# Kernel tuning notes

Hardware: AMD Instinct MI355X
Metric: run time of the kernel (lower is better)

Reference implementation:

```python
import jax, jax.numpy as jnp
import numpy as np

N = 50000      # nodes
C = 64         # in_channels
O = 64         # out_channels (== in_channels, required by zeros_like in original)
S = 8          # size: number of weight matrices
E = 1700000    # edges (neighbor pairs incl. self-loops), avg degree ~34


def setup_inputs() -> dict:
    key = jax.random.key(0)
    ks = jax.random.split(key, 9)
    node_tensor = jax.random.normal(ks[0], (N, C), dtype=jnp.float32)
    src = jax.random.randint(ks[1], (E,), 0, N)                 # neighbor node j
    dst = jnp.sort(jax.random.randint(ks[2], (E,), 0, N))       # center node i
    sc = 1.0 / np.sqrt(C)
    W = jax.random.normal(ks[3], (S, C, O), dtype=jnp.float32) * sc   # linears weights
    b = jax.random.normal(ks[4], (S, O), dtype=jnp.float32) * sc      # linears biases
    Ws = jax.random.normal(ks[5], (C, S), dtype=jnp.float32) * sc     # source proj
    bs = jax.random.normal(ks[6], (S,), dtype=jnp.float32) * sc
    Wt = jax.random.normal(ks[7], (C, S), dtype=jnp.float32) * sc     # target proj
    bt = jax.random.normal(ks[8], (S,), dtype=jnp.float32) * sc
    return dict(node_tensor=node_tensor, src=src, dst=dst,
                W=W, b=b, Ws=Ws, bs=bs, Wt=Wt, bt=bt)


def reference(node_tensor, src, dst, W, b, Ws, bs, Wt, bt):
    # Per-node soft-assignment logits (FeaStNet)
    s = node_tensor @ Ws + bs          # [N, S] : source_tensor
    t = node_tensor @ Wt + bt          # [N, S] : target_tensor
    # Per-edge assignment: softmax over the `size` dim of source[center] + target[neighbor]
    q = jax.nn.softmax(s[dst] + t[src], axis=-1)      # [E, S]
    # Per-matrix projected node features: weighted[m] = x @ W_m + b_m
    Wx = jnp.einsum('nc,sco->sno', node_tensor, W) + b[:, None, :]   # [S, N, O]
    # msg[e] = sum_m q[e,m] * Wx[m, src[e]]; loop over small fixed S to avoid [S,E,O] blowup
    msg = q[:, 0:1] * Wx[0][src]                      # [E, O]
    for m in range(1, S):
        msg = msg + q[:, m:m + 1] * Wx[m][src]
    # Scatter-sum over each center's neighborhood, mean over the S weight matrices
    out = jax.ops.segment_sum(msg, dst, num_segments=N) / S          # [N, O]
    return out
```

## Files before the change

### kernel.cpp

```cpp
#include <hip/hip_runtime.h>
#include <hip/hip_bf16.h>


#define CDIM 64
#define SDIM 8

typedef __bf16 bf16x8 __attribute__((ext_vector_type(8)));
typedef float f32x4 __attribute__((ext_vector_type(4)));

__global__ __launch_bounds__(256) void k1_pre(
    const float* __restrict__ x, const float* __restrict__ Ws,
    const float* __restrict__ bs, const float* __restrict__ Wt,
    const float* __restrict__ bt, const float* __restrict__ W,
    const int* __restrict__ dst, float* __restrict__ ST,
    __hip_bfloat16* __restrict__ xbf, __hip_bfloat16* __restrict__ WtB,
    int* __restrict__ rowptr, int N, int E, int nbN) {
  int bid = blockIdx.x;
  if (bid >= nbN + 128) {
    int e = (bid - nbN - 128) * 256 + threadIdx.x;
    if (e >= E) return;
    int a = dst[e];
    int bnd = (e + 1 < E) ? dst[e + 1] : N;
    if (e == 0) {
      for (int d = 0; d <= a; ++d) rowptr[d] = 0;
    }
    for (int d = a + 1; d <= bnd; ++d) rowptr[d] = e + 1;
    return;
  }
  if (bid >= nbN) {
    int t = (bid - nbN) * 256 + threadIdx.x;
    int o = t >> 9, k = t & 511;
    WtB[t] = __float2bfloat16(W[(size_t)k * 64 + o]);
    return;
  }

  __shared__ __hip_bfloat16 wst[16 * 72];
  __shared__ float bst[16];
  int t = threadIdx.x;
#pragma unroll
  for (int j = 0; j < 4; ++j) {
    int idx = t * 4 + j;
    int n = idx >> 6, k = idx & 63;
    float v = (n < 8) ? Ws[k * 8 + n] : Wt[k * 8 + (n - 8)];
    wst[n * 72 + k] = __float2bfloat16(v);
  }
  if (t < 16) bst[t] = (t < 8) ? bs[t] : bt[t - 8];
  __syncthreads();

  int wave = t >> 6, lane = t & 63;
  int r = lane & 15, q = lane >> 4;
  int node = bid * 64 + wave * 16 + r;
  int nodec = node < N ? node : N - 1;
  const float* xr = x + (size_t)nodec * CDIM;

  bf16x8 afrag[2];
#pragma unroll
  for (int kt = 0; kt < 2; ++kt) {
    float4 u0 = *(const float4*)(xr + kt * 32 + q * 8);
    float4 u1 = *(const float4*)(xr + kt * 32 + q * 8 + 4);
    union { bf16x8 v; __hip_bfloat16 h[8]; } a;
    a.h[0] = __float2bfloat16(u0.x); a.h[1] = __float2bfloat16(u0.y);
    a.h[2] = __float2bfloat16(u0.z); a.h[3] = __float2bfloat16(u0.w);
    a.h[4] = __float2bfloat16(u1.x); a.h[5] = __float2bfloat16(u1.y);
    a.h[6] = __float2bfloat16(u1.z); a.h[7] = __float2bfloat16(u1.w);
    afrag[kt] = a.v;
    if (node < N)
      *(bf16x8*)(xbf + (size_t)node * CDIM + kt * 32 + q * 8) = a.v;
  }

  bf16x8 bf0 = *(const bf16x8*)(wst + r * 72 + q * 8);
  bf16x8 bf1 = *(const bf16x8*)(wst + r * 72 + 32 + q * 8);

  f32x4 acc = {0, 0, 0, 0};
  acc = __builtin_amdgcn_mfma_f32_16x16x32_bf16(afrag[0], bf0, acc, 0, 0, 0);
  acc = __builtin_amdgcn_mfma_f32_16x16x32_bf16(afrag[1], bf1, acc, 0, 0, 0);

  int m = lane & 15;
#pragma unroll
  for (int v = 0; v < 4; ++v) {
    int nd = bid * 64 + wave * 16 + q * 4 + v;
    if (nd >= N) continue;
    float val = acc[v] + bst[m];
    if (m >= 8) val = __expf(val);
    ST[nd * 16 + m] = val;
  }
}

__global__ __launch_bounds__(256) void k3_fused(
    const __hip_bfloat16* __restrict__ xbf, const int* __restrict__ src,
    const int* __restrict__ rowptr, const float* __restrict__ ST,
    __hip_bfloat16* __restrict__ Gbf, float* __restrict__ R, int N) {
  __shared__ float qlds[4][64];
  int wave = __builtin_amdgcn_readfirstlane(threadIdx.x >> 6);
  int lane = threadIdx.x & 63;
  int i = blockIdx.x * 4 + wave;
  if (i >= N) return;

  int lo = rowptr[i];
  int hi = rowptr[i + 1];
  int mm = lane & 7;
  int kk = lane >> 3;

  float uv = __expf(ST[i * 16 + mm]);

  float g[8] = {0, 0, 0, 0, 0, 0, 0, 0};
  float racc = 0.f;
  float* qw = &qlds[wave][0];

  if (lo < hi) {
    int ecl = hi - 1;
    int ek = lo + kk;
    int iv = src[ek < ecl ? ek : ecl];

    for (int e0 = lo; e0 < hi; e0 += 8) {
      int e0n = e0 + 8;
      int ekn = e0n + kk;
      int ivn = (e0n < hi) ? src[ekn < ecl ? ekn : ecl] : iv;

      int j0 = __builtin_amdgcn_readlane(iv, 0);
      int j1 = __builtin_amdgcn_readlane(iv, 8);
      int j2 = __builtin_amdgcn_readlane(iv, 16);
      int j3 = __builtin_amdgcn_readlane(iv, 24);
      int j4 = __builtin_amdgcn_readlane(iv, 32);
      int j5 = __builtin_amdgcn_readlane(iv, 40);
      int j6 = __builtin_amdgcn_readlane(iv, 48);
      int j7 = __builtin_amdgcn_readlane(iv, 56);

      float tv = ST[iv * 16 + 8 + mm];

      float xv[8];
      xv[0] = __bfloat162float(xbf[(size_t)j0 * CDIM + lane]);
      xv[1] = __bfloat162float(xbf[(size_t)j1 * CDIM + lane]);
      xv[2] = __bfloat162float(xbf[(size_t)j2 * CDIM + lane]);
      xv[3] = __bfloat162float(xbf[(size_t)j3 * CDIM + lane]);
      xv[4] = __bfloat162float(xbf[(size_t)j4 * CDIM + lane]);
      xv[5] = __bfloat162float(xbf[(size_t)j5 * CDIM + lane]);
      xv[6] = __bfloat162float(xbf[(size_t)j6 * CDIM + lane]);
      xv[7] = __bfloat162float(xbf[(size_t)j7 * CDIM + lane]);

      float w = uv * tv;
      float ssum = w + __shfl_xor(w, 1);
      ssum += __shfl_xor(ssum, 2);
      ssum += __shfl_xor(ssum, 4);
      float qv = w * __frcp_rn(ssum);
      if (e0 + kk >= hi) qv = 0.f;
      racc += qv;
      qw[lane] = qv;

#pragma unroll
      for (int k = 0; k < 8; ++k) {
        float4 qa = *(const float4*)(qw + k * 8);
        float4 qb = *(const float4*)(qw + k * 8 + 4);
        float xk = xv[k];
        g[0] = fmaf(qa.x, xk, g[0]);
        g[1] = fmaf(qa.y, xk, g[1]);
        g[2] = fmaf(qa.z, xk, g[2]);
        g[3] = fmaf(qa.w, xk, g[3]);
        g[4] = fmaf(qb.x, xk, g[4]);
        g[5] = fmaf(qb.y, xk, g[5]);
        g[6] = fmaf(qb.z, xk, g[6]);
        g[7] = fmaf(qb.w, xk, g[7]);
      }
      iv = ivn;
    }
  }

  __hip_bfloat16* Gi = Gbf + (size_t)i * 512;
#pragma unroll
  for (int m = 0; m < 8; ++m) Gi[m * 64 + lane] = __float2bfloat16(g[m]);

  racc += __shfl_xor(racc, 8);
  racc += __shfl_xor(racc, 16);
  racc += __shfl_xor(racc, 32);
  if (lane < 8) R[(size_t)i * 8 + lane] = racc;
}

__global__ __launch_bounds__(256) void k4_mfma(
    const __hip_bfloat16* __restrict__ Gbf, const float* __restrict__ R,
    const __hip_bfloat16* __restrict__ WtB, const float* __restrict__ bias,
    float* __restrict__ out, int N) {
  __shared__ float4 btile[64 * 65];
  {
    const float4* srcp = (const float4*)WtB;
    int t = threadIdx.x;
#pragma unroll
    for (int j = 0; j < 16; ++j) {
      int ci = t + j * 256;
      btile[(ci >> 6) * 65 + (ci & 63)] = srcp[ci];
    }
  }
  __syncthreads();

  int wave = threadIdx.x >> 6;
  int lane = threadIdx.x & 63;
  int r0 = (blockIdx.x * 4 + wave) * 16;
  if (r0 >= N) return;

  int m = lane & 15;
  int q = lane >> 4;
  const __bf16* abase = (const __bf16*)(Gbf + (size_t)(r0 + m) * 512) + q * 8;
  const __bf16* lbase = (const __bf16*)btile + (size_t)m * 520 + q * 8;

  f32x4 acc0 = {0, 0, 0, 0}, acc1 = {0, 0, 0, 0};
  f32x4 acc2 = {0, 0, 0, 0}, acc3 = {0, 0, 0, 0};
#pragma unroll
  for (int kt = 0; kt < 16; ++kt) {
    bf16x8 a = *(const bf16x8*)(abase + kt * 32);
    bf16x8 b0 = *(const bf16x8*)(lbase + 0 * 520 + kt * 32);
    bf16x8 b1 = *(const bf16x8*)(lbase + 16 * 520 + kt * 32);
    bf16x8 b2 = *(const bf16x8*)(lbase + 32 * 520 + kt * 32);
    bf16x8 b3 = *(const bf16x8*)(lbase + 48 * 520 + kt * 32);
    acc0 = __builtin_amdgcn_mfma_f32_16x16x32_bf16(a, b0, acc0, 0, 0, 0);
    acc1 = __builtin_amdgcn_mfma_f32_16x16x32_bf16(a, b1, acc1, 0, 0, 0);
    acc2 = __builtin_amdgcn_mfma_f32_16x16x32_bf16(a, b2, acc2, 0, 0, 0);
    acc3 = __builtin_amdgcn_mfma_f32_16x16x32_bf16(a, b3, acc3, 0, 0, 0);
  }

#pragma unroll
  for (int v = 0; v < 4; ++v) {
    int ri = r0 + q * 4 + v;
    if (ri >= N) continue;
    const float* Ri = R + (size_t)ri * 8;
    float b0s = 0, b1s = 0, b2s = 0, b3s = 0;
#pragma unroll
    for (int mm = 0; mm < 8; ++mm) {
      float rv = Ri[mm];
      b0s = fmaf(rv, bias[mm * 64 + 0 + m], b0s);
      b1s = fmaf(rv, bias[mm * 64 + 16 + m], b1s);
      b2s = fmaf(rv, bias[mm * 64 + 32 + m], b2s);
      b3s = fmaf(rv, bias[mm * 64 + 48 + m], b3s);
    }
    float* orow = out + (size_t)ri * 64;
    orow[0 + m]  = (acc0[v] + b0s) * 0.125f;
    orow[16 + m] = (acc1[v] + b1s) * 0.125f;
    orow[32 + m] = (acc2[v] + b2s) * 0.125f;
    orow[48 + m] = (acc3[v] + b3s) * 0.125f;
  }
}

extern "C" void kernel_launch(void* const* d_in, const int* in_sizes, int n_in,
                              void* d_out, int out_size, void* d_ws, size_t ws_size,
                              hipStream_t stream) {
  const float* x  = (const float*)d_in[0];
  const int* src  = (const int*)d_in[1];
  const int* dst  = (const int*)d_in[2];
  const float* W  = (const float*)d_in[3];
  const float* b  = (const float*)d_in[4];
  const float* Ws = (const float*)d_in[5];
  const float* bs = (const float*)d_in[6];
  const float* Wt = (const float*)d_in[7];
  const float* bt = (const float*)d_in[8];
  int N = in_sizes[0] / CDIM;
  int E = in_sizes[1];
  float* out = (float*)d_out;

  float* ST = (float*)d_ws;
  __hip_bfloat16* Gbf = (__hip_bfloat16*)(ST + (size_t)N * 16);
  float* R  = (float*)(Gbf + (size_t)N * 512);
  __hip_bfloat16* WtB = (__hip_bfloat16*)(R + (size_t)N * 8);
  __hip_bfloat16* xbf = WtB + 64 * 512;
  int* rowptr = (int*)(xbf + (size_t)N * CDIM);

  int nbN = (N + 63) / 64;
  int nbE = (E + 255) / 256;
  k1_pre<<<nbN + 128 + nbE, 256, 0, stream>>>(x, Ws, bs, Wt, bt, W, dst, ST,
                                              xbf, WtB, rowptr, N, E, nbN);
  k3_fused<<<(N + 3) / 4, 256, 0, stream>>>(xbf, src, rowptr, ST, Gbf, R, N);
  int mtiles = (N + 15) / 16;
  k4_mfma<<<(mtiles + 3) / 4, 256, 0, stream>>>(Gbf, R, WtB, b, out, N);
}
```

Measured before the change: 160.1 us.

## Compute per-node q^T·X aggregation with MFMA over 32-edge chunks

The gather-aggregation kernel now processes 32 edges per iteration. Each lane loads 8 contiguous bf16 channels per neighbor as a vector instead of scalar loads. The q weights and gathered x rows are staged in LDS as bf16 tiles, and the 8x64 per-node product is computed with 16x16x32 bf16 MFMA instead of scalar FMAs. This cuts ALU work and load instruction count, but adds LDS staging, a transposing scalar LDS read, and padding waste for low-degree nodes, with q rounded to bf16.

```diff
diff --git a/kernel.cpp b/kernel.cpp
--- a/kernel.cpp
+++ b/kernel.cpp
@@ -86,88 +86,115 @@
   }
 }
 
-__global__ __launch_bounds__(256) void k3_fused(
+__global__ __launch_bounds__(256) void k3_mfma(
     const __hip_bfloat16* __restrict__ xbf, const int* __restrict__ src,
     const int* __restrict__ rowptr, const float* __restrict__ ST,
     __hip_bfloat16* __restrict__ Gbf, float* __restrict__ R, int N) {
-  __shared__ float qlds[4][64];
-  int wave = __builtin_amdgcn_readfirstlane(threadIdx.x >> 6);
+  __shared__ __hip_bfloat16 qt_s[4][16 * 40];
+  __shared__ __hip_bfloat16 xt_s[4][32 * 72];
+
+  int wave = threadIdx.x >> 6;
   int lane = threadIdx.x & 63;
   int i = blockIdx.x * 4 + wave;
   if (i >= N) return;
 
+  int mm = lane & 7;
+  int kk = lane >> 3;
+  int mp = lane & 15;
+  int q3 = lane >> 4;
+
+  __hip_bfloat16* qt = &qt_s[wave][0];
+  __hip_bfloat16* xt = &xt_s[wave][0];
+
+  __hip_bfloat16 z0 = __float2bfloat16(0.0f);
+#pragma unroll
+  for (int z = 0; z < 5; ++z) qt[320 + z * 64 + lane] = z0;
+
   int lo = rowptr[i];
   int hi = rowptr[i + 1];
-  int mm = lane & 7;
-  int kk = lane >> 3;
-
   float uv = __expf(ST[i * 16 + mm]);
 
-  float g[8] = {0, 0, 0, 0, 0, 0, 0, 0};
+  f32x4 acc0 = {0, 0, 0, 0}, acc1 = {0, 0, 0, 0};
+  f32x4 acc2 = {0, 0, 0, 0}, acc3 = {0, 0, 0, 0};
   float racc = 0.f;
-  float* qw = &qlds[wave][0];
 
   if (lo < hi) {
     int ecl = hi - 1;
-    int ek = lo + kk;
-    int iv = src[ek < ecl ? ek : ecl];
-
-    for (int e0 = lo; e0 < hi; e0 += 8) {
-      int e0n = e0 + 8;
-      int ekn = e0n + kk;
-      int ivn = (e0n < hi) ? src[ekn < ecl ? ekn : ecl] : iv;
-
-      int j0 = __builtin_amdgcn_readlane(iv, 0);
-      int j1 = __builtin_amdgcn_readlane(iv, 8);
-      int j2 = __builtin_amdgcn_readlane(iv, 16);
-      int j3 = __builtin_amdgcn_readlane(iv, 24);
-      int j4 = __builtin_amdgcn_readlane(iv, 32);
-      int j5 = __builtin_amdgcn_readlane(iv, 40);
-      int j6 = __builtin_amdgcn_readlane(iv, 48);
-      int j7 = __builtin_amdgcn_readlane(iv, 56);
-
-      float tv = ST[iv * 16 + 8 + mm];
-
-      float xv[8];
-      xv[0] = __bfloat162float(xbf[(size_t)j0 * CDIM + lane]);
-      xv[1] = __bfloat162float(xbf[(size_t)j1 * CDIM + lane]);
-      xv[2] = __bfloat162float(xbf[(size_t)j2 * CDIM + lane]);
-      xv[3] = __bfloat162float(xbf[(size_t)j3 * CDIM + lane]);
-      xv[4] = __bfloat162float(xbf[(size_t)j4 * CDIM + lane]);
-      xv[5] = __bfloat162float(xbf[(size_t)j5 * CDIM + lane]);
-      xv[6] = __bfloat162float(xbf[(size_t)j6 * CDIM + lane]);
-      xv[7] = __bfloat162float(xbf[(size_t)j7 * CDIM + lane]);
-
-      float w = uv * tv;
-      float ssum = w + __shfl_xor(w, 1);
-      ssum += __shfl_xor(ssum, 2);
-      ssum += __shfl_xor(ssum, 4);
-      float qv = w * __frcp_rn(ssum);
-      if (e0 + kk >= hi) qv = 0.f;
-      racc += qv;
-      qw[lane] = qv;
-
-#pragma unroll
-      for (int k = 0; k < 8; ++k) {
-        float4 qa = *(const float4*)(qw + k * 8);
-        float4 qb = *(const float4*)(qw + k * 8 + 4);
-        float xk = xv[k];
-        g[0] = fmaf(qa.x, xk, g[0]);
-        g[1] = fmaf(qa.y, xk, g[1]);
-        g[2] = fmaf(qa.z, xk, g[2]);
-        g[3] = fmaf(qa.w, xk, g[3]);
-        g[4] = fmaf(qb.x, xk, g[4]);
-        g[5] = fmaf(qb.y, xk, g[5]);
-        g[6] = fmaf(qb.z, xk, g[6]);
-        g[7] = fmaf(qb.w, xk, g[7]);
+    int iv[4];
+#pragma unroll
+    for (int g = 0; g < 4; ++g) {
+      int ek = lo + g * 8 + kk;
+      iv[g] = src[ek < ecl ? ek : ecl];
+    }
+
+    for (int c0 = lo; c0 < hi; c0 += 32) {
+      bf16x8 xv[4];
+#pragma unroll
+      for (int g = 0; g < 4; ++g)
+        xv[g] = *(const bf16x8*)(xbf + (size_t)iv[g] * CDIM + mm * 8);
+
+      float tv[4];
+#pragma unroll
+      for (int g = 0; g < 4; ++g) tv[g] = ST[iv[g] * 16 + 8 + mm];
+
+      int nc0 = c0 + 32;
+      int niv[4];
+#pragma unroll
+      for (int g = 0; g < 4; ++g) {
+        int ek = nc0 + g * 8 + kk;
+        ek = ek < ecl ? ek : ecl;
+        niv[g] = (nc0 < hi) ? src[ek] : iv[g];
       }
-      iv = ivn;
-    }
-  }
-
-  __hip_bfloat16* Gi = Gbf + (size_t)i * 512;
-#pragma unroll
-  for (int m = 0; m < 8; ++m) Gi[m * 64 + lane] = __float2bfloat16(g[m]);
+
+#pragma unroll
+      for (int g = 0; g < 4; ++g) {
+        float w = uv * tv[g];
+        float ssum = w + __shfl_xor(w, 1);
+        ssum += __shfl_xor(ssum, 2);
+        ssum += __shfl_xor(ssum, 4);
+        float qv = w * __frcp_rn(ssum);
+        if (c0 + g * 8 + kk >= hi) qv = 0.f;
+        racc += qv;
+        qt[mm * 40 + g * 8 + kk] = __float2bfloat16(qv);
+      }
+
+#pragma unroll
+      for (int g = 0; g < 4; ++g)
+        *(bf16x8*)(xt + (g * 8 + kk) * 72 + mm * 8) = xv[g];
+
+      bf16x8 afrag = *(const bf16x8*)(qt + mp * 40 + q3 * 8);
+
+      {
+        union { bf16x8 v; __hip_bfloat16 h[8]; } b0, b1, b2, b3;
+#pragma unroll
+        for (int j = 0; j < 8; ++j) {
+          const __hip_bfloat16* xr = xt + (q3 * 8 + j) * 72 + mp;
+          b0.h[j] = xr[0];
+          b1.h[j] = xr[16];
+          b2.h[j] = xr[32];
+          b3.h[j] = xr[48];
+        }
+        acc0 = __builtin_amdgcn_mfma_f32_16x16x32_bf16(afrag, b0.v, acc0, 0, 0, 0);
+        acc1 = __builtin_amdgcn_mfma_f32_16x16x32_bf16(afrag, b1.v, acc1, 0, 0, 0);
+        acc2 = __builtin_amdgcn_mfma_f32_16x16x32_bf16(afrag, b2.v, acc2, 0, 0, 0);
+        acc3 = __builtin_amdgcn_mfma_f32_16x16x32_bf16(afrag, b3.v, acc3, 0, 0, 0);
+      }
+
+      iv[0] = niv[0]; iv[1] = niv[1]; iv[2] = niv[2]; iv[3] = niv[3];
+    }
+  }
+
+  if (q3 < 2) {
+    __hip_bfloat16* Gi = Gbf + (size_t)i * 512;
+#pragma unroll
+    for (int v = 0; v < 4; ++v) {
+      int m = q3 * 4 + v;
+      Gi[m * 64 + 0 + mp]  = __float2bfloat16(acc0[v]);
+      Gi[m * 64 + 16 + mp] = __float2bfloat16(acc1[v]);
+      Gi[m * 64 + 32 + mp] = __float2bfloat16(acc2[v]);
+      Gi[m * 64 + 48 + mp] = __float2bfloat16(acc3[v]);
+    }
+  }
 
   racc += __shfl_xor(racc, 8);
   racc += __shfl_xor(racc, 16);
@@ -265,7 +292,7 @@
   int nbE = (E + 255) / 256;
   k1_pre<<<nbN + 128 + nbE, 256, 0, stream>>>(x, Ws, bs, Wt, bt, W, dst, ST,
                                               xbf, WtB, rowptr, N, E, nbN);
-  k3_fused<<<(N + 3) / 4, 256, 0, stream>>>(xbf, src, rowptr, ST, Gbf, R, N);
+  k3_mfma<<<(N + 3) / 4, 256, 0, stream>>>(xbf, src, rowptr, ST, Gbf, R, N);
   int mtiles = (N + 15) / 16;
   k4_mfma<<<(mtiles + 3) / 4, 256, 0, stream>>>(Gbf, R, WtB, b, out, N);
 }
```

Result: faster. 156.8 us (-2.1%).
